# Optimization experiments

Measured on AMD Instinct MI355X. Metric: run time of the kernel, lower is better.

## Reference

```python
import jax, jax.numpy as jnp
import numpy as np

NUM_EMBEDDINGS = 1024
EMBEDDING_DIM = 64
COMMITMENT_COST = 0.25


def setup_inputs() -> dict:
    key = jax.random.key(0)
    k1, k2 = jax.random.split(key)
    inputs = jax.random.normal(k1, (64, 32, 32, EMBEDDING_DIM), dtype=jnp.float32)
    # torch init is uniform(-1/K, 1/K); scale accordingly
    weight = jax.random.uniform(
        k2, (NUM_EMBEDDINGS, EMBEDDING_DIM), dtype=jnp.float32,
        minval=-1.0 / NUM_EMBEDDINGS, maxval=1.0 / NUM_EMBEDDINGS)
    return {"inputs": inputs, "weight": weight}


def reference(inputs, weight):
    input_shape = inputs.shape
    flat = inputs.reshape(-1, EMBEDDING_DIM)               # [N, D]
    distances = (jnp.sum(flat ** 2, axis=1, keepdims=True)
                 + jnp.sum(weight ** 2, axis=1)
                 - 2.0 * flat @ weight.T)                   # [N, K]
    encoding_indices = jnp.argmin(distances, axis=1)        # [N]
    # gather codes (equivalent to one-hot @ weight, but as a direct gather)
    quantized = weight[encoding_indices].reshape(input_shape)

    e_latent_loss = jnp.mean((jax.lax.stop_gradient(quantized) - inputs) ** 2)
    q_latent_loss = jnp.mean((quantized - jax.lax.stop_gradient(inputs)) ** 2)
    loss = q_latent_loss + COMMITMENT_COST * e_latent_loss

    # straight-through estimator
    quantized_ste = inputs + jax.lax.stop_gradient(quantized - inputs)

    # perplexity (equivalent to mean over the one-hot encodings)
    n_tokens = flat.shape[0]
    counts = jax.ops.segment_sum(
        jnp.ones((n_tokens,), jnp.float32), encoding_indices,
        num_segments=NUM_EMBEDDINGS)
    avg_probs = counts / n_tokens
    perplexity = jnp.exp(-jnp.sum(avg_probs * jnp.log(avg_probs + 1e-10)))

    indices_for_transformer = encoding_indices.reshape(input_shape[0], -1)
    return (loss, quantized_ste, perplexity, indices_for_transformer)
```

## Files before the change

kernel.cpp:

```cpp
#include <hip/hip_runtime.h>
#include <cstdint>
#include <cstddef>

#define N_TOKENS 65536
#define DIM 64
#define K_CODES 1024
#define NTH 256
#define TPB 128
#define NBLK (N_TOKENS / TPB)

#define OFF_Q 1
#define OFF_PERP 4194305
#define OFF_IDX 4194306

#define MARGIN 2.5e-5f
#define XSCALE 1024.0f
#define WSCALE 65536.0f
#define AINIT_SC -33554432.0f
#define D_UNSC  -2.9802322387695312e-08f

#define WS_LOSS   0
#define WS_TICKET 8
#define WS_COUNTS 16
#define WS_WHI    4112
#define WS_WLO    135184
#define WS_S2     266256

typedef _Float16 f16x8 __attribute__((ext_vector_type(8)));
typedef _Float16 f16x4 __attribute__((ext_vector_type(4)));
typedef float    f32x4 __attribute__((ext_vector_type(4)));

__device__ __forceinline__ float fmulr(float a, float b){ return __fmul_rn(a,b); }
__device__ __forceinline__ float faddr(float a, float b){ return __fadd_rn(a,b); }

__device__ __forceinline__ unsigned keyf(float f) {
    unsigned u = __float_as_uint(f);
    return u ^ ((u & 0x80000000u) ? 0xffffffffu : 0x80000000u);
}

__device__ __forceinline__ void split16(float v, _Float16& h, _Float16& l) {
    h = (_Float16)v;
    l = (_Float16)(v - (float)h);
}

__device__ float sumsq64_np(const float* __restrict__ p) {
    float s[16];
    #pragma unroll
    for (int l = 0; l < 16; ++l) {
        float a0 = fmulr(p[l],      p[l]);
        float a1 = fmulr(p[l + 16], p[l + 16]);
        float a2 = fmulr(p[l + 32], p[l + 32]);
        float a3 = fmulr(p[l + 48], p[l + 48]);
        s[l] = faddr(faddr(a0, a1), faddr(a2, a3));
    }
    #pragma unroll
    for (int len = 8; len >= 1; len >>= 1)
        #pragma unroll
        for (int l = 0; l < len; ++l)
            s[l] = faddr(s[l], s[l + len]);
    return s[0];
}

__global__ void vq_prep(const float* __restrict__ W, _Float16* __restrict__ Whi,
                        _Float16* __restrict__ Wlo, float* __restrict__ s2g,
                        int* __restrict__ counts, int* __restrict__ ticket,
                        double* __restrict__ loss_acc) {
    int gid = blockIdx.x * NTH + threadIdx.x;
    if (gid < 16384) {
        f32x4 v = *(const f32x4*)(W + gid * 4);
        f16x4 h, l;
        #pragma unroll
        for (int j = 0; j < 4; ++j) {
            _Float16 hh, ll; split16(v[j] * WSCALE, hh, ll);
            h[j] = hh; l[j] = ll;
        }
        *(f16x4*)(Whi + gid * 4) = h;
        *(f16x4*)(Wlo + gid * 4) = l;
    }
    if (gid < K_CODES) { s2g[gid] = sumsq64_np(W + gid * 64); counts[gid] = 0; }
    if (gid == 0) { *loss_acc = 0.0; *ticket = 0; }
}

__global__ __launch_bounds__(NTH, 2)
void vq_main(const float* __restrict__ X, const float* __restrict__ W,
             const _Float16* __restrict__ WhiG, const _Float16* __restrict__ WloG,
             const float* __restrict__ s2g, float* __restrict__ out,
             double* __restrict__ loss_acc, int* __restrict__ counts,
             int* __restrict__ ticket) {
    __shared__ float m1v[2][TPB];
    __shared__ int   m1i[2][TPB];
    __shared__ float m2v[2][TPB];
    __shared__ int   fidx[TPB];
    __shared__ int   flist[TPB];
    __shared__ int   fcount, lastFlag;
    __shared__ double lred[4];

    const int tid  = threadIdx.x;
    const int lane = tid & 63, wave = tid >> 6;
    const int quad = lane >> 4, lrow = lane & 15;
    const int t0   = blockIdx.x * TPB;
    const int wtok = t0 + (wave >> 1) * 64;
    const int c0   = (wave & 1) * 512;
    const int half = wave & 1;

    if (tid == 0) fcount = 0;

    f16x8 a_h0[4], a_h1[4], a_l0[4], a_l1[4];
    #pragma unroll
    for (int rt = 0; rt < 4; ++rt) {
        const float* xrow = X + (size_t)(wtok + rt * 16 + lrow) * DIM;
        f32x4 v0 = *(const f32x4*)(xrow + quad * 8);
        f32x4 v1 = *(const f32x4*)(xrow + quad * 8 + 4);
        f32x4 v2 = *(const f32x4*)(xrow + 32 + quad * 8);
        f32x4 v3 = *(const f32x4*)(xrow + 32 + quad * 8 + 4);
        #pragma unroll
        for (int j = 0; j < 4; ++j) {
            _Float16 h, l;
            split16(v0[j] * XSCALE, h, l); a_h0[rt][j]     = h; a_l0[rt][j]     = l;
            split16(v1[j] * XSCALE, h, l); a_h0[rt][j + 4] = h; a_l0[rt][j + 4] = l;
            split16(v2[j] * XSCALE, h, l); a_h1[rt][j]     = h; a_l1[rt][j]     = l;
            split16(v3[j] * XSCALE, h, l); a_h1[rt][j + 4] = h; a_l1[rt][j + 4] = l;
        }
    }

    float r1v[16], r2v[16]; int r1i[16];
    #pragma unroll
    for (int ri = 0; ri < 16; ++ri) { r1v[ri] = 3.4e38f; r2v[ri] = 3.4e38f; r1i[ri] = 0x7fffffff; }

    f16x8 bh0[2], bh1[2], bl0[2], bl1[2]; float s2v[2];
    {
        int code = c0 + lrow;
        const _Float16* ph = WhiG + code * 64 + quad * 8;
        const _Float16* pl = WloG + code * 64 + quad * 8;
        bh0[0] = *(const f16x8*)ph; bh1[0] = *(const f16x8*)(ph + 32);
        bl0[0] = *(const f16x8*)pl; bl1[0] = *(const f16x8*)(pl + 32);
        s2v[0] = s2g[code];
    }
    #pragma unroll 2
    for (int tile = 0; tile < 32; ++tile) {
        const int cur = tile & 1;
        if (tile < 31) {
            int code = c0 + (tile + 1) * 16 + lrow;
            const _Float16* ph = WhiG + code * 64 + quad * 8;
            const _Float16* pl = WloG + code * 64 + quad * 8;
            bh0[cur ^ 1] = *(const f16x8*)ph; bh1[cur ^ 1] = *(const f16x8*)(ph + 32);
            bl0[cur ^ 1] = *(const f16x8*)pl; bl1[cur ^ 1] = *(const f16x8*)(pl + 32);
            s2v[cur ^ 1] = s2g[code];
        }
        int jcode = c0 + tile * 16 + lrow;
        float ainit = fmulr(s2v[cur], AINIT_SC);
        #pragma unroll
        for (int rt = 0; rt < 4; ++rt) {
            f32x4 acc = {ainit, ainit, ainit, ainit};
            acc = __builtin_amdgcn_mfma_f32_16x16x32_f16(a_h0[rt], bh0[cur], acc, 0, 0, 0);
            acc = __builtin_amdgcn_mfma_f32_16x16x32_f16(a_h1[rt], bh1[cur], acc, 0, 0, 0);
            acc = __builtin_amdgcn_mfma_f32_16x16x32_f16(a_h0[rt], bl0[cur], acc, 0, 0, 0);
            acc = __builtin_amdgcn_mfma_f32_16x16x32_f16(a_h1[rt], bl1[cur], acc, 0, 0, 0);
            acc = __builtin_amdgcn_mfma_f32_16x16x32_f16(a_l0[rt], bh0[cur], acc, 0, 0, 0);
            acc = __builtin_amdgcn_mfma_f32_16x16x32_f16(a_l1[rt], bh1[cur], acc, 0, 0, 0);
            #pragma unroll
            for (int r = 0; r < 4; ++r) {
                float d = fmulr(acc[r], D_UNSC);
                int ri = rt * 4 + r;
                bool lt = d < r1v[ri];
                float sec = lt ? r1v[ri] : d;
                r2v[ri] = fminf(r2v[ri], sec);
                r1v[ri] = lt ? d : r1v[ri];
                r1i[ri] = lt ? jcode : r1i[ri];
            }
        }
    }

    #pragma unroll
    for (int m = 1; m <= 8; m <<= 1) {
        #pragma unroll
        for (int ri = 0; ri < 16; ++ri) {
            float o1v = __shfl_xor(r1v[ri], m, 64);
            int   o1i = __shfl_xor(r1i[ri], m, 64);
            float o2v = __shfl_xor(r2v[ri], m, 64);
            bool take = (o1v < r1v[ri]) || (o1v == r1v[ri] && o1i < r1i[ri]);
            float loser = take ? r1v[ri] : o1v;
            r2v[ri] = fminf(fminf(r2v[ri], o2v), loser);
            if (take) { r1v[ri] = o1v; r1i[ri] = o1i; }
        }
    }
    if (lrow == 0) {
        #pragma unroll
        for (int ri = 0; ri < 16; ++ri) {
            int rt = ri >> 2, r = ri & 3;
            int tloc = (wave >> 1) * 64 + rt * 16 + quad * 4 + r;
            m1v[half][tloc] = r1v[ri];
            m1i[half][tloc] = r1i[ri];
            m2v[half][tloc] = r2v[ri];
        }
    }
    __syncthreads();

    if (tid < TPB) {
        float v0 = m1v[0][tid], v1 = m1v[1][tid];
        bool t1 = v1 < v0;
        float b1v = t1 ? v1 : v0;
        int   b1i = t1 ? m1i[1][tid] : m1i[0][tid];
        float loser = t1 ? v0 : v1;
        float b2v = fminf(fminf(m2v[0][tid], m2v[1][tid]), loser);
        bool fb = (b2v - b1v) < MARGIN;
        fidx[tid] = fb ? (b1i | (int)0x80000000) : b1i;
        if (fb) { int p = atomicAdd(&fcount, 1); flist[p] = tid; }
    }
    __syncthreads();

    double lsum = 0.0;
    #pragma unroll
    for (int i = 0; i < 8; ++i) {
        int e4 = tid + NTH * i;
        int t = e4 >> 4, d4 = (e4 & 15) * 4;
        int iv = fidx[t];
        if (iv >= 0) {
            f32x4 q = *(const f32x4*)&W[iv * 64 + d4];
            f32x4 x = *(const f32x4*)&X[(size_t)(t0 + t) * 64 + d4];
            *(f32x4*)&out[(size_t)OFF_Q + (size_t)(t0 + t) * 64 + d4] = q;
            #pragma unroll
            for (int c = 0; c < 4; ++c) {
                float df = __fsub_rn(q[c], x[c]);
                lsum += (double)fmulr(df, df);
            }
        }
    }
    #pragma unroll
    for (int off = 32; off >= 1; off >>= 1) lsum += __shfl_down(lsum, off, 64);
    if (lane == 0) lred[wave] = lsum;
    if (tid < TPB) {
        int iv = fidx[tid];
        if (iv >= 0) {
            atomicAdd(&counts[iv], 1);
            out[(size_t)OFF_IDX + t0 + tid] = (float)iv;
        }
    }
    __syncthreads();
    if (tid == 0) atomicAdd(loss_acc, lred[0] + lred[1] + lred[2] + lred[3]);

    for (int fi = wave; fi < fcount; fi += 4) {
        int t = flist[fi];
        int gtok = t0 + t;
        float s1v = sumsq64_np(X + (size_t)gtok * 64);
        f32x4 xr[16];
        #pragma unroll
        for (int kb = 0; kb < 16; ++kb)
            xr[kb] = *(const f32x4*)(X + (size_t)gtok * 64 + kb * 4);
        unsigned long long best = ~0ULL;
        #pragma unroll 1
        for (int c16 = 0; c16 < 16; ++c16) {
            int code = lane * 16 + c16;
            const float* wr = W + code * 64;
            float acc = 0.0f;
            #pragma unroll
            for (int kb = 0; kb < 16; ++kb) {
                f32x4 wv = *(const f32x4*)(wr + kb * 4);
                acc = __builtin_fmaf(xr[kb][0], wv[0], acc);
                acc = __builtin_fmaf(xr[kb][1], wv[1], acc);
                acc = __builtin_fmaf(xr[kb][2], wv[2], acc);
                acc = __builtin_fmaf(xr[kb][3], wv[3], acc);
            }
            float d = faddr(faddr(s1v, s2g[code]), fmulr(-2.0f, acc));
            unsigned long long pk = ((unsigned long long)keyf(d) << 32) | (unsigned)code;
            best = pk < best ? pk : best;
        }
        #pragma unroll
        for (int m = 32; m >= 1; m >>= 1) {
            unsigned long long o = __shfl_xor(best, m, 64);
            best = o < best ? o : best;
        }
        int idx = (int)(best & 0xffffffffu);
        float q = W[idx * 64 + lane];
        float x = X[(size_t)gtok * 64 + lane];
        out[(size_t)OFF_Q + (size_t)gtok * 64 + lane] = q;
        float df = __fsub_rn(q, x);
        double ls = (double)fmulr(df, df);
        #pragma unroll
        for (int m = 32; m >= 1; m >>= 1) ls += __shfl_xor(ls, m, 64);
        if (lane == 0) {
            out[(size_t)OFF_IDX + gtok] = (float)idx;
            atomicAdd(&counts[idx], 1);
            atomicAdd(loss_acc, ls);
        }
    }

    __syncthreads();
    if (tid == 0) {
        __threadfence();
        int old = atomicAdd(ticket, 1);
        lastFlag = (old == NBLK - 1) ? 1 : 0;
    }
    __syncthreads();
    if (lastFlag) {
        double h = 0.0;
        for (int j = tid; j < K_CODES; j += NTH) {
            int c = atomicAdd(&counts[j], 0);
            double p = (double)c / 65536.0;
            h += p * log(p + 1e-10);
        }
        #pragma unroll
        for (int off = 32; off >= 1; off >>= 1) h += __shfl_down(h, off, 64);
        if (lane == 0) lred[wave] = h;
        __syncthreads();
        if (tid == 0) {
            double H = lred[0] + lred[1] + lred[2] + lred[3];
            out[OFF_PERP] = (float)exp(-H);
            double ls = atomicAdd(loss_acc, 0.0);
            float Lf = (float)(ls / 4194304.0);
            out[0] = faddr(Lf, fmulr(0.25f, Lf));
        }
    }
}

extern "C" void kernel_launch(void* const* d_in, const int* in_sizes, int n_in,
                              void* d_out, int out_size, void* d_ws, size_t ws_size,
                              hipStream_t stream) {
    const float* X = (const float*)d_in[0];
    const float* W = (const float*)d_in[1];
    float* out = (float*)d_out;
    char* ws = (char*)d_ws;
    double* loss_acc = (double*)(ws + WS_LOSS);
    int* ticket = (int*)(ws + WS_TICKET);
    int* counts = (int*)(ws + WS_COUNTS);
    _Float16* Whi = (_Float16*)(ws + WS_WHI);
    _Float16* Wlo = (_Float16*)(ws + WS_WLO);
    float* s2g = (float*)(ws + WS_S2);

    vq_prep<<<128, NTH, 0, stream>>>(W, Whi, Wlo, s2g, counts, ticket, loss_acc);
    vq_main<<<NBLK, NTH, 0, stream>>>(X, W, Whi, Wlo, s2g, out,
                                      loss_acc, counts, ticket);
}
```

Baseline: 187.1 us.

## Halve tokens per block and split codebook four ways across waves

Each block now handles 64 tokens instead of 128. All four waves share the same token rows, and each wave scans a quarter of the codebook (256 codes) instead of half. The inner loop processes two 16-code tiles per iteration, with all MFMAs issued before the argmin updates, which gives more independent MFMA chains for latency hiding. This doubles the grid size but loads each W tile into more blocks, so codebook traffic goes up and the cross-wave merge reads four partial results instead of two.

```diff
diff --git a/kernel.cpp b/kernel.cpp
--- a/kernel.cpp
+++ b/kernel.cpp
@@ -6,7 +6,7 @@
 #define DIM 64
 #define K_CODES 1024
 #define NTH 256
-#define TPB 128
+#define TPB 64
 #define NBLK (N_TOKENS / TPB)
 
 #define OFF_Q 1
@@ -87,9 +87,9 @@
              const float* __restrict__ s2g, float* __restrict__ out,
              double* __restrict__ loss_acc, int* __restrict__ counts,
              int* __restrict__ ticket) {
-    __shared__ float m1v[2][TPB];
-    __shared__ int   m1i[2][TPB];
-    __shared__ float m2v[2][TPB];
+    __shared__ float m1v[4][TPB];
+    __shared__ int   m1i[4][TPB];
+    __shared__ float m2v[4][TPB];
     __shared__ int   fidx[TPB];
     __shared__ int   flist[TPB];
     __shared__ int   fcount, lastFlag;
@@ -99,16 +99,14 @@
     const int lane = tid & 63, wave = tid >> 6;
     const int quad = lane >> 4, lrow = lane & 15;
     const int t0   = blockIdx.x * TPB;
-    const int wtok = t0 + (wave >> 1) * 64;
-    const int c0   = (wave & 1) * 512;
-    const int half = wave & 1;
+    const int c0   = wave * 256;
 
     if (tid == 0) fcount = 0;
 
     f16x8 a_h0[4], a_h1[4], a_l0[4], a_l1[4];
     #pragma unroll
     for (int rt = 0; rt < 4; ++rt) {
-        const float* xrow = X + (size_t)(wtok + rt * 16 + lrow) * DIM;
+        const float* xrow = X + (size_t)(t0 + rt * 16 + lrow) * DIM;
         f32x4 v0 = *(const f32x4*)(xrow + quad * 8);
         f32x4 v1 = *(const f32x4*)(xrow + quad * 8 + 4);
         f32x4 v2 = *(const f32x4*)(xrow + 32 + quad * 8);
@@ -127,46 +125,60 @@
     #pragma unroll
     for (int ri = 0; ri < 16; ++ri) { r1v[ri] = 3.4e38f; r2v[ri] = 3.4e38f; r1i[ri] = 0x7fffffff; }
 
-    f16x8 bh0[2], bh1[2], bl0[2], bl1[2]; float s2v[2];
-    {
-        int code = c0 + lrow;
+    f16x8 bh0[2][2], bh1[2][2], bl0[2][2], bl1[2][2]; float s2v[2][2];
+    #pragma unroll
+    for (int ct = 0; ct < 2; ++ct) {
+        int code = c0 + ct * 16 + lrow;
         const _Float16* ph = WhiG + code * 64 + quad * 8;
         const _Float16* pl = WloG + code * 64 + quad * 8;
-        bh0[0] = *(const f16x8*)ph; bh1[0] = *(const f16x8*)(ph + 32);
-        bl0[0] = *(const f16x8*)pl; bl1[0] = *(const f16x8*)(pl + 32);
-        s2v[0] = s2g[code];
+        bh0[0][ct] = *(const f16x8*)ph; bh1[0][ct] = *(const f16x8*)(ph + 32);
+        bl0[0][ct] = *(const f16x8*)pl; bl1[0][ct] = *(const f16x8*)(pl + 32);
+        s2v[0][ct] = s2g[code];
     }
     #pragma unroll 2
-    for (int tile = 0; tile < 32; ++tile) {
-        const int cur = tile & 1;
-        if (tile < 31) {
-            int code = c0 + (tile + 1) * 16 + lrow;
-            const _Float16* ph = WhiG + code * 64 + quad * 8;
-            const _Float16* pl = WloG + code * 64 + quad * 8;
-            bh0[cur ^ 1] = *(const f16x8*)ph; bh1[cur ^ 1] = *(const f16x8*)(ph + 32);
-            bl0[cur ^ 1] = *(const f16x8*)pl; bl1[cur ^ 1] = *(const f16x8*)(pl + 32);
-            s2v[cur ^ 1] = s2g[code];
-        }
-        int jcode = c0 + tile * 16 + lrow;
-        float ainit = fmulr(s2v[cur], AINIT_SC);
-        #pragma unroll
-        for (int rt = 0; rt < 4; ++rt) {
-            f32x4 acc = {ainit, ainit, ainit, ainit};
-            acc = __builtin_amdgcn_mfma_f32_16x16x32_f16(a_h0[rt], bh0[cur], acc, 0, 0, 0);
-            acc = __builtin_amdgcn_mfma_f32_16x16x32_f16(a_h1[rt], bh1[cur], acc, 0, 0, 0);
-            acc = __builtin_amdgcn_mfma_f32_16x16x32_f16(a_h0[rt], bl0[cur], acc, 0, 0, 0);
-            acc = __builtin_amdgcn_mfma_f32_16x16x32_f16(a_h1[rt], bl1[cur], acc, 0, 0, 0);
-            acc = __builtin_amdgcn_mfma_f32_16x16x32_f16(a_l0[rt], bh0[cur], acc, 0, 0, 0);
-            acc = __builtin_amdgcn_mfma_f32_16x16x32_f16(a_l1[rt], bh1[cur], acc, 0, 0, 0);
-            #pragma unroll
-            for (int r = 0; r < 4; ++r) {
-                float d = fmulr(acc[r], D_UNSC);
-                int ri = rt * 4 + r;
-                bool lt = d < r1v[ri];
-                float sec = lt ? r1v[ri] : d;
-                r2v[ri] = fminf(r2v[ri], sec);
-                r1v[ri] = lt ? d : r1v[ri];
-                r1i[ri] = lt ? jcode : r1i[ri];
+    for (int g = 0; g < 8; ++g) {
+        const int cur = g & 1;
+        if (g < 7) {
+            #pragma unroll
+            for (int ct = 0; ct < 2; ++ct) {
+                int code = c0 + (g + 1) * 32 + ct * 16 + lrow;
+                const _Float16* ph = WhiG + code * 64 + quad * 8;
+                const _Float16* pl = WloG + code * 64 + quad * 8;
+                bh0[cur ^ 1][ct] = *(const f16x8*)ph; bh1[cur ^ 1][ct] = *(const f16x8*)(ph + 32);
+                bl0[cur ^ 1][ct] = *(const f16x8*)pl; bl1[cur ^ 1][ct] = *(const f16x8*)(pl + 32);
+                s2v[cur ^ 1][ct] = s2g[code];
+            }
+        }
+        f32x4 acc[2][4];
+        #pragma unroll
+        for (int ct = 0; ct < 2; ++ct) {
+            float ainit = fmulr(s2v[cur][ct], AINIT_SC);
+            #pragma unroll
+            for (int rt = 0; rt < 4; ++rt) {
+                f32x4 a = {ainit, ainit, ainit, ainit};
+                a = __builtin_amdgcn_mfma_f32_16x16x32_f16(a_h0[rt], bh0[cur][ct], a, 0, 0, 0);
+                a = __builtin_amdgcn_mfma_f32_16x16x32_f16(a_h1[rt], bh1[cur][ct], a, 0, 0, 0);
+                a = __builtin_amdgcn_mfma_f32_16x16x32_f16(a_h0[rt], bl0[cur][ct], a, 0, 0, 0);
+                a = __builtin_amdgcn_mfma_f32_16x16x32_f16(a_h1[rt], bl1[cur][ct], a, 0, 0, 0);
+                a = __builtin_amdgcn_mfma_f32_16x16x32_f16(a_l0[rt], bh0[cur][ct], a, 0, 0, 0);
+                a = __builtin_amdgcn_mfma_f32_16x16x32_f16(a_l1[rt], bh1[cur][ct], a, 0, 0, 0);
+                acc[ct][rt] = a;
+            }
+        }
+        #pragma unroll
+        for (int ct = 0; ct < 2; ++ct) {
+            int jc = c0 + g * 32 + ct * 16 + lrow;
+            #pragma unroll
+            for (int rt = 0; rt < 4; ++rt) {
+                #pragma unroll
+                for (int r = 0; r < 4; ++r) {
+                    float d = fmulr(acc[ct][rt][r], D_UNSC);
+                    int ri = rt * 4 + r;
+                    bool lt = d < r1v[ri];
+                    r2v[ri] = fminf(r2v[ri], fmaxf(d, r1v[ri]));
+                    r1v[ri] = lt ? d : r1v[ri];
+                    r1i[ri] = lt ? jc : r1i[ri];
+                }
             }
         }
     }
@@ -188,21 +200,25 @@
         #pragma unroll
         for (int ri = 0; ri < 16; ++ri) {
             int rt = ri >> 2, r = ri & 3;
-            int tloc = (wave >> 1) * 64 + rt * 16 + quad * 4 + r;
-            m1v[half][tloc] = r1v[ri];
-            m1i[half][tloc] = r1i[ri];
-            m2v[half][tloc] = r2v[ri];
+            int tloc = rt * 16 + quad * 4 + r;
+            m1v[wave][tloc] = r1v[ri];
+            m1i[wave][tloc] = r1i[ri];
+            m2v[wave][tloc] = r2v[ri];
         }
     }
     __syncthreads();
 
     if (tid < TPB) {
-        float v0 = m1v[0][tid], v1 = m1v[1][tid];
-        bool t1 = v1 < v0;
-        float b1v = t1 ? v1 : v0;
-        int   b1i = t1 ? m1i[1][tid] : m1i[0][tid];
-        float loser = t1 ? v0 : v1;
-        float b2v = fminf(fminf(m2v[0][tid], m2v[1][tid]), loser);
+        float b1v = m1v[0][tid]; int b1i = m1i[0][tid]; float b2v = m2v[0][tid];
+        #pragma unroll
+        for (int q = 1; q < 4; ++q) {
+            float v = m1v[q][tid];
+            bool take = v < b1v;
+            float loser = take ? b1v : v;
+            b2v = fminf(fminf(b2v, m2v[q][tid]), loser);
+            b1v = take ? v : b1v;
+            b1i = take ? m1i[q][tid] : b1i;
+        }
         bool fb = (b2v - b1v) < MARGIN;
         fidx[tid] = fb ? (b1i | (int)0x80000000) : b1i;
         if (fb) { int p = atomicAdd(&fcount, 1); flist[p] = tid; }
@@ -211,7 +227,7 @@
 
     double lsum = 0.0;
     #pragma unroll
-    for (int i = 0; i < 8; ++i) {
+    for (int i = 0; i < 4; ++i) {
         int e4 = tid + NTH * i;
         int t = e4 >> 4, d4 = (e4 & 15) * 4;
         int iv = fidx[t];
```

Result: slower. 195.1 us (+4.3%).

## Halve tokens per block to cut registers and raise occupancy

Applied to the files above, without the earlier changes.

Each block now covers 64 tokens instead of 128, so each wave holds 2 row tiles of A fragments and running-min state instead of 4, and launch bounds ask for 4 blocks per CU instead of 2. The MFMA chains for the two row tiles are issued together before the argmin update, and the second-min update becomes a fminf/fmaxf pair. The goal is more waves in flight to hide the codebook loads and MFMA latency, and more blocks to fill the device. The cost is that each codebook tile loaded from global/L2 now feeds half as many MFMAs, so codebook traffic per token doubles.

```diff
diff --git a/kernel.cpp b/kernel.cpp
--- a/kernel.cpp
+++ b/kernel.cpp
@@ -6,7 +6,7 @@
 #define DIM 64
 #define K_CODES 1024
 #define NTH 256
-#define TPB 128
+#define TPB 64
 #define NBLK (N_TOKENS / TPB)
 
 #define OFF_Q 1
@@ -81,7 +81,7 @@
     if (gid == 0) { *loss_acc = 0.0; *ticket = 0; }
 }
 
-__global__ __launch_bounds__(NTH, 2)
+__global__ __launch_bounds__(NTH, 4)
 void vq_main(const float* __restrict__ X, const float* __restrict__ W,
              const _Float16* __restrict__ WhiG, const _Float16* __restrict__ WloG,
              const float* __restrict__ s2g, float* __restrict__ out,
@@ -99,15 +99,16 @@
     const int lane = tid & 63, wave = tid >> 6;
     const int quad = lane >> 4, lrow = lane & 15;
     const int t0   = blockIdx.x * TPB;
-    const int wtok = t0 + (wave >> 1) * 64;
-    const int c0   = (wave & 1) * 512;
-    const int half = wave & 1;
+    const int th   = wave >> 1;
+    const int chf  = wave & 1;
+    const int c0   = chf * 512;
+    const int wtok = t0 + th * 32;
 
     if (tid == 0) fcount = 0;
 
-    f16x8 a_h0[4], a_h1[4], a_l0[4], a_l1[4];
-    #pragma unroll
-    for (int rt = 0; rt < 4; ++rt) {
+    f16x8 a_h0[2], a_h1[2], a_l0[2], a_l1[2];
+    #pragma unroll
+    for (int rt = 0; rt < 2; ++rt) {
         const float* xrow = X + (size_t)(wtok + rt * 16 + lrow) * DIM;
         f32x4 v0 = *(const f32x4*)(xrow + quad * 8);
         f32x4 v1 = *(const f32x4*)(xrow + quad * 8 + 4);
@@ -123,9 +124,9 @@
         }
     }
 
-    float r1v[16], r2v[16]; int r1i[16];
-    #pragma unroll
-    for (int ri = 0; ri < 16; ++ri) { r1v[ri] = 3.4e38f; r2v[ri] = 3.4e38f; r1i[ri] = 0x7fffffff; }
+    float r1v[8], r2v[8]; int r1i[8];
+    #pragma unroll
+    for (int ri = 0; ri < 8; ++ri) { r1v[ri] = 3.4e38f; r2v[ri] = 3.4e38f; r1i[ri] = 0x7fffffff; }
 
     f16x8 bh0[2], bh1[2], bl0[2], bl1[2]; float s2v[2];
     {
@@ -147,24 +148,28 @@
             bl0[cur ^ 1] = *(const f16x8*)pl; bl1[cur ^ 1] = *(const f16x8*)(pl + 32);
             s2v[cur ^ 1] = s2g[code];
         }
+        float ainit = fmulr(s2v[cur], AINIT_SC);
+        f32x4 acc[2];
+        #pragma unroll
+        for (int rt = 0; rt < 2; ++rt) {
+            f32x4 a = {ainit, ainit, ainit, ainit};
+            a = __builtin_amdgcn_mfma_f32_16x16x32_f16(a_h0[rt], bh0[cur], a, 0, 0, 0);
+            a = __builtin_amdgcn_mfma_f32_16x16x32_f16(a_h1[rt], bh1[cur], a, 0, 0, 0);
+            a = __builtin_amdgcn_mfma_f32_16x16x32_f16(a_h0[rt], bl0[cur], a, 0, 0, 0);
+            a = __builtin_amdgcn_mfma_f32_16x16x32_f16(a_h1[rt], bl1[cur], a, 0, 0, 0);
+            a = __builtin_amdgcn_mfma_f32_16x16x32_f16(a_l0[rt], bh0[cur], a, 0, 0, 0);
+            a = __builtin_amdgcn_mfma_f32_16x16x32_f16(a_l1[rt], bh1[cur], a, 0, 0, 0);
+            acc[rt] = a;
+        }
         int jcode = c0 + tile * 16 + lrow;
-        float ainit = fmulr(s2v[cur], AINIT_SC);
-        #pragma unroll
-        for (int rt = 0; rt < 4; ++rt) {
-            f32x4 acc = {ainit, ainit, ainit, ainit};
-            acc = __builtin_amdgcn_mfma_f32_16x16x32_f16(a_h0[rt], bh0[cur], acc, 0, 0, 0);
-            acc = __builtin_amdgcn_mfma_f32_16x16x32_f16(a_h1[rt], bh1[cur], acc, 0, 0, 0);
-            acc = __builtin_amdgcn_mfma_f32_16x16x32_f16(a_h0[rt], bl0[cur], acc, 0, 0, 0);
-            acc = __builtin_amdgcn_mfma_f32_16x16x32_f16(a_h1[rt], bl1[cur], acc, 0, 0, 0);
-            acc = __builtin_amdgcn_mfma_f32_16x16x32_f16(a_l0[rt], bh0[cur], acc, 0, 0, 0);
-            acc = __builtin_amdgcn_mfma_f32_16x16x32_f16(a_l1[rt], bh1[cur], acc, 0, 0, 0);
+        #pragma unroll
+        for (int rt = 0; rt < 2; ++rt) {
             #pragma unroll
             for (int r = 0; r < 4; ++r) {
-                float d = fmulr(acc[r], D_UNSC);
+                float d = fmulr(acc[rt][r], D_UNSC);
                 int ri = rt * 4 + r;
                 bool lt = d < r1v[ri];
-                float sec = lt ? r1v[ri] : d;
-                r2v[ri] = fminf(r2v[ri], sec);
+                r2v[ri] = fminf(r2v[ri], fmaxf(d, r1v[ri]));
                 r1v[ri] = lt ? d : r1v[ri];
                 r1i[ri] = lt ? jcode : r1i[ri];
             }
@@ -174,7 +179,7 @@
     #pragma unroll
     for (int m = 1; m <= 8; m <<= 1) {
         #pragma unroll
-        for (int ri = 0; ri < 16; ++ri) {
+        for (int ri = 0; ri < 8; ++ri) {
             float o1v = __shfl_xor(r1v[ri], m, 64);
             int   o1i = __shfl_xor(r1i[ri], m, 64);
             float o2v = __shfl_xor(r2v[ri], m, 64);
@@ -186,12 +191,12 @@
     }
     if (lrow == 0) {
         #pragma unroll
-        for (int ri = 0; ri < 16; ++ri) {
+        for (int ri = 0; ri < 8; ++ri) {
             int rt = ri >> 2, r = ri & 3;
-            int tloc = (wave >> 1) * 64 + rt * 16 + quad * 4 + r;
-            m1v[half][tloc] = r1v[ri];
-            m1i[half][tloc] = r1i[ri];
-            m2v[half][tloc] = r2v[ri];
+            int tloc = th * 32 + rt * 16 + quad * 4 + r;
+            m1v[chf][tloc] = r1v[ri];
+            m1i[chf][tloc] = r1i[ri];
+            m2v[chf][tloc] = r2v[ri];
         }
     }
     __syncthreads();
@@ -211,7 +216,7 @@
 
     double lsum = 0.0;
     #pragma unroll
-    for (int i = 0; i < 8; ++i) {
+    for (int i = 0; i < 4; ++i) {
         int e4 = tid + NTH * i;
         int t = e4 >> 4, d4 = (e4 & 15) * 4;
         int iv = fidx[t];
```

New measurement: 201.9 us. 1.08x slower.
